# Optimization experiments

Hardware: AMD Instinct MI355X
Metric: run time of the kernel (lower is better)

Reference implementation:

```python
import jax, jax.numpy as jnp
import numpy as np

B, N, M, DN, DE, WN, WE, P = 16, 128, 1024, 512, 256, 128, 128, 512
EMB = WN + WE            # nenn embedding size per node / per edge
CLS_IN = 2 * EMB // 1    # = 2*wn + 2*we = 512
LR_OUT, CR_OUT, MR_OUT = 9, 6, 17
HID = 256


def _mk_params(key):
    ks = jax.random.split(key, 16)
    s = 0.02
    p = {
        'Wn':  jax.random.normal(ks[0], (DN, WN), jnp.float32) * s,
        'We':  jax.random.normal(ks[1], (DE, WE), jnp.float32) * s,
        'Wn2': jax.random.normal(ks[2], (DN, WN), jnp.float32) * s,
        'We2': jax.random.normal(ks[3], (DE, WE), jnp.float32) * s,
    }
    for i, h in enumerate(['scr', 'lr', 'mr']):
        out = {'scr': CR_OUT, 'lr': LR_OUT, 'mr': MR_OUT}[h]
        p[h + '_W1'] = jax.random.normal(ks[4 + 4 * i], (2 * EMB, HID), jnp.float32) * s
        p[h + '_b1'] = jnp.zeros((HID,), jnp.float32)
        p[h + '_W2'] = jax.random.normal(ks[5 + 4 * i], (HID, out), jnp.float32) * s
        p[h + '_b2'] = jnp.zeros((out,), jnp.float32)
    return p


def setup_inputs() -> dict:
    key = jax.random.key(0)
    ks = jax.random.split(key, 10)
    inp = {
        'node_features': jax.random.normal(ks[0], (B, N, DN), jnp.float32),
        'edge_features': jax.random.normal(ks[1], (B, N, N, DE), jnp.float32),
        'adj_mat': (jax.random.uniform(ks[2], (B, N, N)) < 0.1).astype(jnp.float32),
        'line_adj_mat': (jax.random.uniform(ks[3], (B, M, M)) < 0.02).astype(jnp.float32),
        'edge_index': jax.random.randint(ks[4], (B, 2, M), 0, N, jnp.int32),
        'object_pairs': jax.random.randint(ks[5], (B, P, 2), 0, N, jnp.int32),
        'num_obj': jax.random.randint(ks[6], (B,), N // 4, N + 1, jnp.int32),
        'num_edges': jax.random.randint(ks[7], (B,), M // 4, M + 1, jnp.int32),
    }
    inp.update(_mk_params(ks[8]))
    return inp


def _mlp(x, W1, b1, W2, b2):
    return jax.nn.relu(x @ W1 + b1) @ W2 + b2


def _forward(node_features, edge_features, adj_mat, line_adj_mat,
             Wn, We, Wn2, We2,
             scr_W1, scr_b1, scr_W2, scr_b2,
             lr_W1, lr_b1, lr_W2, lr_b2,
             mr_W1, mr_b1, mr_W2, mr_b2,
             edge_index, object_pairs, num_obj, num_edges):
    dt = node_features.dtype
    # ragged slicing [:num_obj] / [:num_edges] expressed as masks (padding stays 0)
    nmask = (jnp.arange(N) < num_obj[:, None]).astype(dt)      # [B,N]
    emask = (jnp.arange(M) < num_edges[:, None]).astype(dt)    # [B,M]

    X = node_features * nmask[..., None]                        # [B,N,DN]
    A = (adj_mat * nmask[:, :, None] * nmask[:, None, :]
         + jnp.eye(N, dtype=dt)[None] * nmask[:, :, None])      # A + I, masked
    h = jax.nn.relu((A @ X) @ Wn) * nmask[..., None]            # [B,N,WN] node-level emb

    src, dst = edge_index[:, 0], edge_index[:, 1]               # [B,M]
    Eg = jax.vmap(lambda e, s, d: e[s, d])(edge_features, src, dst)  # [B,M,DE]
    Eg = Eg * emask[..., None]
    L = (line_adj_mat * emask[:, :, None] * emask[:, None, :]
         + jnp.eye(M, dtype=dt)[None] * emask[:, :, None])      # line graph A + I
    g = jax.nn.relu((L @ Eg) @ We) * emask[..., None]           # [B,M,WE] edge-level emb

    # aggregate edge embeddings onto their source nodes (ragged scatter-add)
    agg = jax.vmap(lambda gb, sb: jnp.zeros((N, WE), gb.dtype).at[sb].add(gb))(g, src)
    node_emb = jnp.concatenate([h, agg * nmask[..., None]], -1)  # [B,N,EMB]

    # dense pairwise edge embeddings [B,N,N,EMB]
    Xp = X @ Wn2                                                 # [B,N,WN]
    Pm = jax.nn.relu(Xp[:, :, None, :] + Xp[:, None, :, :])      # node part [B,N,N,WN]
    Q = jax.nn.relu(edge_features @ We2)                         # edge part [B,N,N,WE]
    edge_emb = jnp.concatenate([Pm, Q], -1)

    # make_classifier_inputs: fused ragged gather instead of python double loop
    p0, p1 = object_pairs[..., 0], object_pairs[..., 1]          # [B,P]
    emb0 = jnp.take_along_axis(node_emb, p0[:, :, None], axis=1)  # [B,P,EMB]
    emb1 = jnp.take_along_axis(node_emb, p1[:, :, None], axis=1)
    eedge = jax.vmap(lambda eb, a, b: eb[a, b])(edge_emb, p0, p1)  # [B,P,EMB]
    ci = jnp.concatenate([emb0 + emb1, eedge], -1)               # aggregator='sum'

    lr = _mlp(ci, lr_W1, lr_b1, lr_W2, lr_b2)
    cr = _mlp(ci, scr_W1, scr_b1, scr_W2, scr_b2)
    mr = _mlp(ci, mr_W1, mr_b1, mr_W2, mr_b2)
    return lr, cr, mr


def reference(node_features, edge_features, adj_mat, line_adj_mat,
              edge_index, object_pairs, num_obj, num_edges,
              Wn, We, Wn2, We2,
              scr_W1, scr_b1, scr_W2, scr_b2,
              lr_W1, lr_b1, lr_W2, lr_b2,
              mr_W1, mr_b1, mr_W2, mr_b2):
    return _forward(node_features, edge_features, adj_mat, line_adj_mat,
                    Wn, We, Wn2, We2,
                    scr_W1, scr_b1, scr_W2, scr_b2,
                    lr_W1, lr_b1, lr_W2, lr_b2,
                    mr_W1, mr_b1, mr_W2, mr_b2,
                    edge_index, object_pairs, num_obj, num_edges)
```

## Files before the change

kernel.cpp:

```cpp
#include <hip/hip_runtime.h>
#include <hip/hip_bf16.h>
#include <cstdint>
#include <cstddef>

#define BB 16
#define NN 128
#define MM 1024
#define DN 512
#define DE 256
#define WN 128
#define WE 128
#define PP 512
#define HIDW 256
#define CIW 512

typedef __attribute__((ext_vector_type(8))) short s16x8;
typedef __attribute__((ext_vector_type(4))) float f32x4;

__device__ __forceinline__ float bf2f(unsigned short u) {
    unsigned int x = ((unsigned int)u) << 16;
    union { unsigned int i; float f; } c; c.i = x; return c.f;
}
__device__ __forceinline__ short f2b(float f) {
    __hip_bfloat16 h = __float2bfloat16(f);
    return *reinterpret_cast<short*>(&h);
}

__global__ __launch_bounds__(256) void k0_prep(
    const float* __restrict__ lrW1, const float* __restrict__ scrW1,
    const float* __restrict__ mrW1,
    const float* __restrict__ lrb1, const float* __restrict__ scrb1,
    const float* __restrict__ mrb1,
    const float* __restrict__ Wn, const float* __restrict__ Wn2,
    const float* __restrict__ We, const float* __restrict__ We2,
    __hip_bfloat16* __restrict__ W1t, __hip_bfloat16* __restrict__ WncT,
    __hip_bfloat16* __restrict__ WeT, __hip_bfloat16* __restrict__ We2T,
    float* __restrict__ b1cat)
{
    int blk = blockIdx.x;
    int t = threadIdx.x;
    if (blk < 768) {
        int h = blk >> 8, n = blk & 255;
        const float* W = (h == 0) ? lrW1 : (h == 1) ? scrW1 : mrW1;
        W1t[(size_t)blk * 512 + t]       = __float2bfloat16(W[t * 256 + n]);
        W1t[(size_t)blk * 512 + t + 256] = __float2bfloat16(W[(t + 256) * 256 + n]);
    } else if (blk == 768) {
        b1cat[t]       = lrb1[t];
        b1cat[256 + t] = scrb1[t];
        b1cat[512 + t] = mrb1[t];
    } else if (blk < 897) {
        int n = blk - 769;
        WeT[(size_t)n * 256 + t] = __float2bfloat16(We[t * 128 + n]);
    } else if (blk < 1153) {
        int n = blk - 897;
        const float* W = (n < 128) ? Wn : Wn2;
        int c = n & 127;
        WncT[(size_t)n * 512 + t]       = __float2bfloat16(W[t * 128 + c]);
        WncT[(size_t)n * 512 + t + 256] = __float2bfloat16(W[(t + 256) * 128 + c]);
    } else {
        int n = blk - 1153;
        We2T[(size_t)n * 256 + t] = __float2bfloat16(We2[t * 128 + n]);
    }
}

__global__ __launch_bounds__(256) void fproj(
    const float* __restrict__ nf, const float* __restrict__ ef,
    const int* __restrict__ eidx, const int* __restrict__ opair,
    const int* __restrict__ nobj, const int* __restrict__ nedg,
    const ushort* __restrict__ WncT, const ushort* __restrict__ WeT,
    const ushort* __restrict__ We2T,
    float* __restrict__ Y, float* __restrict__ Xp,
    float* __restrict__ G1, __hip_bfloat16* __restrict__ ci)
{
    __shared__ ushort As[128 * 32];
    __shared__ ushort Bs[128 * 32];
    __shared__ unsigned rowoff[128];
    __shared__ float    rowval[128];

    int blk = blockIdx.x;
    int route, mb, nb, K;
    const ushort* Bt;
    if (blk < 32)       { route = 0; mb = blk >> 1;  nb = blk & 1; K = 512; Bt = WncT; }
    else if (blk < 160) { route = 1; mb = blk - 32;  nb = 0;       K = 256; Bt = WeT;  }
    else                { route = 2; mb = blk - 160; nb = 0;       K = 256; Bt = We2T; }
    int row0 = mb * 128, col0 = nb * 128;
    int t = threadIdx.x;

    if (t < 128) {
        int r = row0 + t;
        unsigned off; float valid = 1.f;
        if (route == 0) {
            int b = r >> 7, i = r & 127;
            off = (unsigned)r * DN;
            valid = (i < nobj[b]) ? 1.f : 0.f;
        } else if (route == 1) {
            int b = r >> 10, m = r & 1023;
            int src = eidx[b * 2 * MM + m];
            int dst = eidx[b * 2 * MM + MM + m];
            off = (unsigned)((b * NN + src) * NN + dst) * DE;
            valid = (m < nedg[b]) ? 1.f : 0.f;
        } else {
            int r2 = r;
            int b = r2 >> 9, p = r2 & 511;
            int i0 = opair[(b * PP + p) * 2];
            int i1 = opair[(b * PP + p) * 2 + 1];
            off = (unsigned)((b * NN + i0) * NN + i1) * DE;
        }
        rowoff[t] = off; rowval[t] = valid;
    }

    const float* Asrc = (route == 0) ? nf : ef;
    int lane = t & 63;
    int w    = t >> 6;
    int wr   = w >> 1, wc = w & 1;
    int arow = w * 32 + (lane >> 2);
    int ak   = (lane & 3) * 8;
    int qk   = (lane >> 4) * 8;
    int fr   = lane & 15;
    f32x4 acc[4][4];
    #pragma unroll
    for (int i = 0; i < 4; ++i)
        #pragma unroll
        for (int j = 0; j < 4; ++j) acc[i][j] = (f32x4){0.f, 0.f, 0.f, 0.f};

    for (int k0 = 0; k0 < K; k0 += 32) {
        __syncthreads();
        {
            unsigned o0 = rowoff[arow] + k0 + ak;
            unsigned o1 = rowoff[arow + 16] + k0 + ak;
            float m0 = rowval[arow], m1 = rowval[arow + 16];
            float4 a0 = *(const float4*)&Asrc[o0];
            float4 a1 = *(const float4*)&Asrc[o0 + 4];
            float4 b0 = *(const float4*)&Asrc[o1];
            float4 b1 = *(const float4*)&Asrc[o1 + 4];
            s16x8 pa, pb;
            pa[0]=f2b(a0.x*m0); pa[1]=f2b(a0.y*m0); pa[2]=f2b(a0.z*m0); pa[3]=f2b(a0.w*m0);
            pa[4]=f2b(a1.x*m0); pa[5]=f2b(a1.y*m0); pa[6]=f2b(a1.z*m0); pa[7]=f2b(a1.w*m0);
            pb[0]=f2b(b0.x*m1); pb[1]=f2b(b0.y*m1); pb[2]=f2b(b0.z*m1); pb[3]=f2b(b0.w*m1);
            pb[4]=f2b(b1.x*m1); pb[5]=f2b(b1.y*m1); pb[6]=f2b(b1.z*m1); pb[7]=f2b(b1.w*m1);
            *(s16x8*)&As[arow * 32 + ak]        = pa;
            *(s16x8*)&As[(arow + 16) * 32 + ak] = pb;
            *(s16x8*)&Bs[arow * 32 + ak] =
                *(const s16x8*)&Bt[(size_t)(col0 + arow) * K + k0 + ak];
            *(s16x8*)&Bs[(arow + 16) * 32 + ak] =
                *(const s16x8*)&Bt[(size_t)(col0 + arow + 16) * K + k0 + ak];
        }
        __syncthreads();
        s16x8 af[4], bfv[4];
        #pragma unroll
        for (int mi = 0; mi < 4; ++mi)
            af[mi] = *(const s16x8*)&As[(wr * 64 + mi * 16 + fr) * 32 + qk];
        #pragma unroll
        for (int ni = 0; ni < 4; ++ni)
            bfv[ni] = *(const s16x8*)&Bs[(wc * 64 + ni * 16 + fr) * 32 + qk];
        #pragma unroll
        for (int mi = 0; mi < 4; ++mi)
            #pragma unroll
            for (int ni = 0; ni < 4; ++ni)
                acc[mi][ni] = __builtin_amdgcn_mfma_f32_16x16x32_bf16(
                    af[mi], bfv[ni], acc[mi][ni], 0, 0, 0);
    }
    int crow = (lane >> 4) * 4;
    #pragma unroll
    for (int mi = 0; mi < 4; ++mi) {
        #pragma unroll
        for (int ni = 0; ni < 4; ++ni) {
            int gc = col0 + wc * 64 + ni * 16 + fr;
            int gr = row0 + wr * 64 + mi * 16 + crow;
            #pragma unroll
            for (int rg = 0; rg < 4; ++rg) {
                float v = acc[mi][ni][rg];
                int r = gr + rg;
                if (route == 0) {
                    if (gc < 128) Y [(size_t)r * WN + gc]       = v;
                    else          Xp[(size_t)r * WN + gc - 128] = v;
                } else if (route == 1) {
                    G1[(size_t)r * WE + gc] = v;
                } else {
                    ci[(size_t)r * CIW + 384 + gc] = __float2bfloat16(fmaxf(v, 0.f));
                }
            }
        }
    }
}

__global__ __launch_bounds__(256) void k2_gcn_node(
    const float* __restrict__ adj, const int* __restrict__ num_obj,
    const float* __restrict__ Y, float* __restrict__ node_emb)
{
    __shared__ float As[16 * 129];
    int b  = blockIdx.x >> 4;
    int i0 = ((blockIdx.x >> 1) & 7) * 16;
    int ch = blockIdx.x & 1;
    int s  = num_obj[b];
    int t  = threadIdx.x;
    if (t < 128) {
        for (int rr = 0; rr < 16; ++rr) {
            int i = i0 + rr;
            float v = 0.f;
            if (i < s) {
                v = adj[(size_t)(b * NN + i) * NN + t] * ((t < s) ? 1.f : 0.f);
                if (t == i) v += 1.f;
            }
            As[rr * 129 + t] = v;
        }
    }
    __syncthreads();
    int c  = ch * 64 + (t & 63);
    int rb = (t >> 6) * 4;
    float acc[4] = {0.f,0.f,0.f,0.f};
    for (int j = 0; j < NN; ++j) {
        float yv = Y[(b * NN + j) * WN + c];
        #pragma unroll
        for (int r = 0; r < 4; ++r) acc[r] += As[(rb + r) * 129 + j] * yv;
    }
    #pragma unroll
    for (int r = 0; r < 4; ++r) {
        int i = i0 + rb + r;
        node_emb[(b * NN + i) * 256 + c]       = fmaxf(acc[r], 0.f);
        node_emb[(b * NN + i) * 256 + 128 + c] = 0.f;
    }
}

__global__ __launch_bounds__(128) void k4_line_gcn(
    const float* __restrict__ la, const float* __restrict__ G1,
    const int* __restrict__ eidx, const int* __restrict__ num_edges,
    float* __restrict__ node_emb)
{
    int b = blockIdx.x >> 10;
    int m = blockIdx.x & 1023;
    int se = num_edges[b];
    if (m >= se) return;
    __shared__ int   cnt;
    __shared__ int   idxs[MM];
    __shared__ float vals[MM];
    int t = threadIdx.x;
    if (t == 0) cnt = 0;
    __syncthreads();
    const float* larow = la + ((size_t)b * MM + m) * MM;
    for (int it = 0; it < 8; ++it) {
        int j = it * 128 + t;
        float v = larow[j];
        if (v != 0.f) {
            int pos = atomicAdd(&cnt, 1);
            idxs[pos] = j;
            vals[pos] = v;
        }
    }
    __syncthreads();
    int n = cnt;
    const float* g1b = G1 + (size_t)b * MM * WE;
    float acc = g1b[m * WE + t];
    for (int p = 0; p < n; ++p)
        acc += vals[p] * g1b[idxs[p] * WE + t];
    float g = fmaxf(acc, 0.f);
    int src = eidx[b * 2 * MM + m];
    atomicAdd(&node_emb[(b * NN + src) * 256 + 128 + t], g);
}

__global__ __launch_bounds__(256) void k5a_build_ci(
    const float* __restrict__ node_emb, const float* __restrict__ Xp,
    const int* __restrict__ opairs, const int* __restrict__ num_obj,
    __hip_bfloat16* __restrict__ ci)
{
    __shared__ int   pi0[16], pi1[16];
    __shared__ float nm0[16], nm1[16];
    int b     = blockIdx.x >> 5;
    int pbase = (blockIdx.x & 31) * 16;
    int t     = threadIdx.x;
    int s     = num_obj[b];
    if (t < 16) {
        int p  = pbase + t;
        int i0 = opairs[(b * PP + p) * 2];
        int i1 = opairs[(b * PP + p) * 2 + 1];
        pi0[t] = i0; pi1[t] = i1;
        nm0[t] = (i0 < s) ? 1.f : 0.f;
        nm1[t] = (i1 < s) ? 1.f : 0.f;
    }
    __syncthreads();
    for (int pp = 0; pp < 16; ++pp) {
        int i0 = pi0[pp], i1 = pi1[pp];
        int p  = pbase + pp;
        __hip_bfloat16* cirow = ci + (size_t)(b * PP + p) * CIW;
        float m0f = (t < 128) ? 1.f : nm0[pp];
        float m1f = (t < 128) ? 1.f : nm1[pp];
        float v = node_emb[(b * NN + i0) * 256 + t] * m0f
                + node_emb[(b * NN + i1) * 256 + t] * m1f;
        cirow[t] = __float2bfloat16(v);
        if (t < 128) {
            float pm = Xp[(b * NN + i0) * WN + t] + Xp[(b * NN + i1) * WN + t];
            cirow[256 + t] = __float2bfloat16(fmaxf(pm, 0.f));
        }
    }
}

__global__ __launch_bounds__(256) void k6_mlp1_mfma(
    const ushort* __restrict__ A,
    const ushort* __restrict__ Bt,
    const float* __restrict__ b1cat,
    __hip_bfloat16* __restrict__ H)
{
    __shared__ ushort As[128 * 32];
    __shared__ ushort Bs[128 * 32];
    int t    = threadIdx.x;
    int col0 = blockIdx.x * 128;
    int row0 = blockIdx.y * 128;
    int lane = t & 63;
    int w    = t >> 6;
    int wr   = w >> 1, wc = w & 1;
    int arow = w * 32 + (lane >> 2);
    int ak   = (lane & 3) * 8;
    int qk   = (lane >> 4) * 8;
    int fr   = lane & 15;
    f32x4 acc[4][4];
    #pragma unroll
    for (int i = 0; i < 4; ++i)
        #pragma unroll
        for (int j = 0; j < 4; ++j) acc[i][j] = (f32x4){0.f, 0.f, 0.f, 0.f};

    for (int k0 = 0; k0 < CIW; k0 += 32) {
        __syncthreads();
        *(s16x8*)&As[arow * 32 + ak] =
            *(const s16x8*)&A[(size_t)(row0 + arow) * CIW + k0 + ak];
        *(s16x8*)&As[(arow + 16) * 32 + ak] =
            *(const s16x8*)&A[(size_t)(row0 + arow + 16) * CIW + k0 + ak];
        *(s16x8*)&Bs[arow * 32 + ak] =
            *(const s16x8*)&Bt[(size_t)(col0 + arow) * CIW + k0 + ak];
        *(s16x8*)&Bs[(arow + 16) * 32 + ak] =
            *(const s16x8*)&Bt[(size_t)(col0 + arow + 16) * CIW + k0 + ak];
        __syncthreads();
        s16x8 af[4], bfv[4];
        #pragma unroll
        for (int mi = 0; mi < 4; ++mi)
            af[mi] = *(const s16x8*)&As[(wr * 64 + mi * 16 + fr) * 32 + qk];
        #pragma unroll
        for (int ni = 0; ni < 4; ++ni)
            bfv[ni] = *(const s16x8*)&Bs[(wc * 64 + ni * 16 + fr) * 32 + qk];
        #pragma unroll
        for (int mi = 0; mi < 4; ++mi)
            #pragma unroll
            for (int ni = 0; ni < 4; ++ni)
                acc[mi][ni] = __builtin_amdgcn_mfma_f32_16x16x32_bf16(
                    af[mi], bfv[ni], acc[mi][ni], 0, 0, 0);
    }
    int crow = (lane >> 4) * 4;
    #pragma unroll
    for (int mi = 0; mi < 4; ++mi) {
        #pragma unroll
        for (int ni = 0; ni < 4; ++ni) {
            int gc = col0 + wc * 64 + ni * 16 + fr;
            int gr = row0 + wr * 64 + mi * 16 + crow;
            float bias = b1cat[gc];
            #pragma unroll
            for (int rg = 0; rg < 4; ++rg) {
                float v = fmaxf(acc[mi][ni][rg] + bias, 0.f);
                H[(size_t)(gr + rg) * 768 + gc] = __float2bfloat16(v);
            }
        }
    }
}

__global__ __launch_bounds__(256) void k7_mlp2(
    const __hip_bfloat16* __restrict__ H,
    const float* __restrict__ lrW2, const float* __restrict__ lrb2,
    const float* __restrict__ scrW2, const float* __restrict__ scrb2,
    const float* __restrict__ mrW2, const float* __restrict__ mrb2,
    float* __restrict__ outp)
{
    __shared__ float w2s[32 * 257];
    int t = threadIdx.x;
    for (int o = 0; o < 32; ++o) {
        float v;
        if (o < 9)       v = lrW2[t * 9 + o];
        else if (o < 15) v = scrW2[t * 6 + (o - 9)];
        else             v = mrW2[t * 17 + (o - 15)];
        w2s[o * 257 + t] = v;
    }
    __syncthreads();
    int p = blockIdx.x * 8 + (t >> 5);
    int o = t & 31;
    int seg = (o < 9) ? 0 : ((o < 15) ? 1 : 2);
    const ushort* hr = (const ushort*)H + (size_t)p * 768 + seg * 256;
    const float* wr = &w2s[o * 257];
    float acc = (o < 9) ? lrb2[o] : ((o < 15) ? scrb2[o - 9] : mrb2[o - 15]);
    for (int k = 0; k < HIDW; k += 2) {
        ushort2 u = *(const ushort2*)&hr[k];
        acc += bf2f(u.x) * wr[k] + bf2f(u.y) * wr[k + 1];
    }
    if (o < 9)       outp[(size_t)p * 9 + o] = acc;
    else if (o < 15) outp[8192 * 9 + (size_t)p * 6 + (o - 9)] = acc;
    else             outp[8192 * 15 + (size_t)p * 17 + (o - 15)] = acc;
}

extern "C" void kernel_launch(void* const* d_in, const int* in_sizes, int n_in,
                              void* d_out, int out_size, void* d_ws, size_t ws_size,
                              hipStream_t stream) {
    const float* nf    = (const float*)d_in[0];
    const float* ef    = (const float*)d_in[1];
    const float* adj   = (const float*)d_in[2];
    const float* la    = (const float*)d_in[3];
    const int*   eidx  = (const int*)d_in[4];
    const int*   opair = (const int*)d_in[5];
    const int*   nobj  = (const int*)d_in[6];
    const int*   nedg  = (const int*)d_in[7];
    const float* Wn    = (const float*)d_in[8];
    const float* We    = (const float*)d_in[9];
    const float* Wn2   = (const float*)d_in[10];
    const float* We2   = (const float*)d_in[11];
    const float* scrW1 = (const float*)d_in[12];
    const float* scrb1 = (const float*)d_in[13];
    const float* scrW2 = (const float*)d_in[14];
    const float* scrb2 = (const float*)d_in[15];
    const float* lrW1  = (const float*)d_in[16];
    const float* lrb1  = (const float*)d_in[17];
    const float* lrW2  = (const float*)d_in[18];
    const float* lrb2  = (const float*)d_in[19];
    const float* mrW1  = (const float*)d_in[20];
    const float* mrb1  = (const float*)d_in[21];
    const float* mrW2  = (const float*)d_in[22];
    const float* mrb2  = (const float*)d_in[23];

    float* ws = (float*)d_ws;
    float* Y        = ws;
    float* Xp       = Y + 262144;
    float* node_emb = Xp + 262144;
    float* G1       = node_emb + 524288;
    float* base     = G1 + 2097152;
    __hip_bfloat16* ci   = (__hip_bfloat16*)base;
    __hip_bfloat16* hid  = (__hip_bfloat16*)(base + 2097152);
    __hip_bfloat16* W1t  = (__hip_bfloat16*)(base + 2097152 + 3145728);
    __hip_bfloat16* WncT = (__hip_bfloat16*)(base + 2097152 + 3145728 + 196608);
    __hip_bfloat16* WeT  = (__hip_bfloat16*)(base + 2097152 + 3145728 + 196608 + 65536);
    __hip_bfloat16* We2T = (__hip_bfloat16*)(base + 2097152 + 3145728 + 196608 + 65536 + 16384);
    float* b1cat = base + 2097152 + 3145728 + 196608 + 65536 + 16384 + 16384;

    k0_prep <<<1281, 256, 0, stream>>>(lrW1, scrW1, mrW1, lrb1, scrb1, mrb1,
                                       Wn, Wn2, We, We2,
                                       W1t, WncT, WeT, We2T, b1cat);
    fproj   <<<224, 256, 0, stream>>>(nf, ef, eidx, opair, nobj, nedg,
                                      (const ushort*)WncT, (const ushort*)WeT,
                                      (const ushort*)We2T, Y, Xp, G1, ci);
    k2_gcn_node <<<BB * 8 * 2, 256, 0, stream>>>(adj, nobj, Y, node_emb);
    k4_line_gcn <<<BB * MM, 128, 0, stream>>>(la, G1, eidx, nedg, node_emb);
    k5a_build_ci<<<BB * (PP / 16), 256, 0, stream>>>(node_emb, Xp, opair, nobj, ci);
    k6_mlp1_mfma<<<dim3(6, 64), 256, 0, stream>>>((const ushort*)ci,
                                                  (const ushort*)W1t, b1cat, hid);
    k7_mlp2     <<<8192 / 8, 256, 0, stream>>>(hid, lrW2, lrb2, scrW2, scrb2,
                                               mrW2, mrb2, (float*)d_out);
}
```

Before: 475.0 us.

## Move GCN, line-GCN and MLP2 onto bf16 MFMA and fuse ci build into MLP1

The node GCN and the line-graph GCN become dense bf16 MFMA GEMMs over the adjacency matrices, with masking and self-loops applied while loading tiles. This replaces the per-edge sparse gather loop, which launched 16K blocks. The pair-feature construction (k5a) is folded into the MLP1 A-tile loader, and the second MLP layer becomes an MFMA GEMM against a padded concatenated W2. Intermediates Y and G1 are stored transposed in bf16. The costs are dense work on a sparse line adjacency (1024x1024 per batch) and extra bf16 rounding of the adjacency values and intermediates.

```diff
diff --git a/kernel.cpp b/kernel.cpp
--- a/kernel.cpp
+++ b/kernel.cpp
@@ -8,22 +8,15 @@
 #define MM 1024
 #define DN 512
 #define DE 256
-#define WN 128
-#define WE 128
 #define PP 512
-#define HIDW 256
-#define CIW 512
 
 typedef __attribute__((ext_vector_type(8))) short s16x8;
 typedef __attribute__((ext_vector_type(4))) float f32x4;
-
-__device__ __forceinline__ float bf2f(unsigned short u) {
-    unsigned int x = ((unsigned int)u) << 16;
-    union { unsigned int i; float f; } c; c.i = x; return c.f;
-}
-__device__ __forceinline__ short f2b(float f) {
+typedef __attribute__((ext_vector_type(4))) unsigned short u16x4;
+
+__device__ __forceinline__ unsigned short f2b(float f) {
     __hip_bfloat16 h = __float2bfloat16(f);
-    return *reinterpret_cast<short*>(&h);
+    return *reinterpret_cast<unsigned short*>(&h);
 }
 
 __global__ __launch_bounds__(256) void k0_prep(
@@ -33,33 +26,52 @@
     const float* __restrict__ mrb1,
     const float* __restrict__ Wn, const float* __restrict__ Wn2,
     const float* __restrict__ We, const float* __restrict__ We2,
-    __hip_bfloat16* __restrict__ W1t, __hip_bfloat16* __restrict__ WncT,
-    __hip_bfloat16* __restrict__ WeT, __hip_bfloat16* __restrict__ We2T,
-    float* __restrict__ b1cat)
+    const float* __restrict__ lrW2, const float* __restrict__ scrW2,
+    const float* __restrict__ mrW2,
+    const float* __restrict__ lrb2, const float* __restrict__ scrb2,
+    const float* __restrict__ mrb2,
+    ushort* __restrict__ W1t, ushort* __restrict__ WncT,
+    ushort* __restrict__ WeT, ushort* __restrict__ We2T,
+    ushort* __restrict__ W2catB,
+    float* __restrict__ b1cat, float* __restrict__ b2cat)
 {
     int blk = blockIdx.x;
     int t = threadIdx.x;
     if (blk < 768) {
         int h = blk >> 8, n = blk & 255;
         const float* W = (h == 0) ? lrW1 : (h == 1) ? scrW1 : mrW1;
-        W1t[(size_t)blk * 512 + t]       = __float2bfloat16(W[t * 256 + n]);
-        W1t[(size_t)blk * 512 + t + 256] = __float2bfloat16(W[(t + 256) * 256 + n]);
+        W1t[(size_t)blk * 512 + t]       = f2b(W[t * 256 + n]);
+        W1t[(size_t)blk * 512 + t + 256] = f2b(W[(t + 256) * 256 + n]);
     } else if (blk == 768) {
         b1cat[t]       = lrb1[t];
         b1cat[256 + t] = scrb1[t];
         b1cat[512 + t] = mrb1[t];
     } else if (blk < 897) {
         int n = blk - 769;
-        WeT[(size_t)n * 256 + t] = __float2bfloat16(We[t * 128 + n]);
+        WeT[(size_t)n * 256 + t] = f2b(We[t * 128 + n]);
     } else if (blk < 1153) {
         int n = blk - 897;
         const float* W = (n < 128) ? Wn : Wn2;
         int c = n & 127;
-        WncT[(size_t)n * 512 + t]       = __float2bfloat16(W[t * 128 + c]);
-        WncT[(size_t)n * 512 + t + 256] = __float2bfloat16(W[(t + 256) * 128 + c]);
+        WncT[(size_t)n * 512 + t]       = f2b(W[t * 128 + c]);
+        WncT[(size_t)n * 512 + t + 256] = f2b(W[(t + 256) * 128 + c]);
+    } else if (blk < 1281) {
+        int n = blk - 1153;
+        We2T[(size_t)n * 256 + t] = f2b(We2[t * 128 + n]);
+    } else if (blk < 1313) {
+        int o = blk - 1281;
+        for (int i = 0; i < 3; ++i) {
+            int k = i * 256 + t;
+            int seg = k >> 8, kk = k & 255;
+            float v = 0.f;
+            if (o < 9)       { if (seg == 0) v = lrW2[kk * 9 + o]; }
+            else if (o < 15) { if (seg == 1) v = scrW2[kk * 6 + (o - 9)]; }
+            else             { if (seg == 2) v = mrW2[kk * 17 + (o - 15)]; }
+            W2catB[(size_t)o * 768 + k] = f2b(v);
+        }
     } else {
-        int n = blk - 1153;
-        We2T[(size_t)n * 256 + t] = __float2bfloat16(We2[t * 128 + n]);
+        if (t < 32)
+            b2cat[t] = (t < 9) ? lrb2[t] : (t < 15) ? scrb2[t - 9] : mrb2[t - 15];
     }
 }
 
@@ -69,8 +81,8 @@
     const int* __restrict__ nobj, const int* __restrict__ nedg,
     const ushort* __restrict__ WncT, const ushort* __restrict__ WeT,
     const ushort* __restrict__ We2T,
-    float* __restrict__ Y, float* __restrict__ Xp,
-    float* __restrict__ G1, __hip_bfloat16* __restrict__ ci)
+    ushort* __restrict__ Yt, float* __restrict__ Xp,
+    ushort* __restrict__ G1t, ushort* __restrict__ ci2)
 {
     __shared__ ushort As[128 * 32];
     __shared__ ushort Bs[128 * 32];
@@ -100,8 +112,7 @@
             off = (unsigned)((b * NN + src) * NN + dst) * DE;
             valid = (m < nedg[b]) ? 1.f : 0.f;
         } else {
-            int r2 = r;
-            int b = r2 >> 9, p = r2 & 511;
+            int b = r >> 9, p = r & 511;
             int i0 = opair[(b * PP + p) * 2];
             int i1 = opair[(b * PP + p) * 2 + 1];
             off = (unsigned)((b * NN + i0) * NN + i1) * DE;
@@ -165,169 +176,261 @@
     for (int mi = 0; mi < 4; ++mi) {
         #pragma unroll
         for (int ni = 0; ni < 4; ++ni) {
-            int gc = col0 + wc * 64 + ni * 16 + fr;
-            int gr = row0 + wr * 64 + mi * 16 + crow;
-            #pragma unroll
-            for (int rg = 0; rg < 4; ++rg) {
-                float v = acc[mi][ni][rg];
-                int r = gr + rg;
-                if (route == 0) {
-                    if (gc < 128) Y [(size_t)r * WN + gc]       = v;
-                    else          Xp[(size_t)r * WN + gc - 128] = v;
-                } else if (route == 1) {
-                    G1[(size_t)r * WE + gc] = v;
-                } else {
-                    ci[(size_t)r * CIW + 384 + gc] = __float2bfloat16(fmaxf(v, 0.f));
-                }
+            int c   = wc * 64 + ni * 16 + fr;
+            int lr0 = wr * 64 + mi * 16 + crow;
+            if (route == 0 && nb == 0) {
+                u16x4 pk;
+                #pragma unroll
+                for (int rg = 0; rg < 4; ++rg) pk[rg] = f2b(acc[mi][ni][rg]);
+                *(u16x4*)&Yt[(size_t)mb * 16384 + c * 128 + lr0] = pk;
+            } else if (route == 0) {
+                #pragma unroll
+                for (int rg = 0; rg < 4; ++rg)
+                    Xp[(size_t)(row0 + lr0 + rg) * 128 + c] = acc[mi][ni][rg];
+            } else if (route == 1) {
+                int r0 = row0 + lr0;
+                int b1 = r0 >> 10, m0 = r0 & 1023;
+                u16x4 pk;
+                #pragma unroll
+                for (int rg = 0; rg < 4; ++rg) pk[rg] = f2b(acc[mi][ni][rg]);
+                *(u16x4*)&G1t[(size_t)b1 * 131072 + c * 1024 + m0] = pk;
+            } else {
+                #pragma unroll
+                for (int rg = 0; rg < 4; ++rg)
+                    ci2[(size_t)(row0 + lr0 + rg) * 128 + c] =
+                        f2b(fmaxf(acc[mi][ni][rg], 0.f));
             }
         }
     }
 }
 
-__global__ __launch_bounds__(256) void k2_gcn_node(
-    const float* __restrict__ adj, const int* __restrict__ num_obj,
-    const float* __restrict__ Y, float* __restrict__ node_emb)
-{
-    __shared__ float As[16 * 129];
-    int b  = blockIdx.x >> 4;
-    int i0 = ((blockIdx.x >> 1) & 7) * 16;
-    int ch = blockIdx.x & 1;
-    int s  = num_obj[b];
-    int t  = threadIdx.x;
-    if (t < 128) {
-        for (int rr = 0; rr < 16; ++rr) {
-            int i = i0 + rr;
-            float v = 0.f;
-            if (i < s) {
-                v = adj[(size_t)(b * NN + i) * NN + t] * ((t < s) ? 1.f : 0.f);
-                if (t == i) v += 1.f;
-            }
-            As[rr * 129 + t] = v;
-        }
-    }
-    __syncthreads();
-    int c  = ch * 64 + (t & 63);
-    int rb = (t >> 6) * 4;
-    float acc[4] = {0.f,0.f,0.f,0.f};
-    for (int j = 0; j < NN; ++j) {
-        float yv = Y[(b * NN + j) * WN + c];
-        #pragma unroll
-        for (int r = 0; r < 4; ++r) acc[r] += As[(rb + r) * 129 + j] * yv;
-    }
-    #pragma unroll
-    for (int r = 0; r < 4; ++r) {
-        int i = i0 + rb + r;
-        node_emb[(b * NN + i) * 256 + c]       = fmaxf(acc[r], 0.f);
-        node_emb[(b * NN + i) * 256 + 128 + c] = 0.f;
-    }
-}
-
-__global__ __launch_bounds__(128) void k4_line_gcn(
-    const float* __restrict__ la, const float* __restrict__ G1,
-    const int* __restrict__ eidx, const int* __restrict__ num_edges,
-    float* __restrict__ node_emb)
-{
-    int b = blockIdx.x >> 10;
-    int m = blockIdx.x & 1023;
-    int se = num_edges[b];
-    if (m >= se) return;
-    __shared__ int   cnt;
-    __shared__ int   idxs[MM];
-    __shared__ float vals[MM];
-    int t = threadIdx.x;
-    if (t == 0) cnt = 0;
-    __syncthreads();
-    const float* larow = la + ((size_t)b * MM + m) * MM;
-    for (int it = 0; it < 8; ++it) {
-        int j = it * 128 + t;
-        float v = larow[j];
-        if (v != 0.f) {
-            int pos = atomicAdd(&cnt, 1);
-            idxs[pos] = j;
-            vals[pos] = v;
-        }
-    }
-    __syncthreads();
-    int n = cnt;
-    const float* g1b = G1 + (size_t)b * MM * WE;
-    float acc = g1b[m * WE + t];
-    for (int p = 0; p < n; ++p)
-        acc += vals[p] * g1b[idxs[p] * WE + t];
-    float g = fmaxf(acc, 0.f);
-    int src = eidx[b * 2 * MM + m];
-    atomicAdd(&node_emb[(b * NN + src) * 256 + 128 + t], g);
-}
-
-__global__ __launch_bounds__(256) void k5a_build_ci(
-    const float* __restrict__ node_emb, const float* __restrict__ Xp,
-    const int* __restrict__ opairs, const int* __restrict__ num_obj,
-    __hip_bfloat16* __restrict__ ci)
-{
-    __shared__ int   pi0[16], pi1[16];
-    __shared__ float nm0[16], nm1[16];
-    int b     = blockIdx.x >> 5;
-    int pbase = (blockIdx.x & 31) * 16;
-    int t     = threadIdx.x;
-    int s     = num_obj[b];
-    if (t < 16) {
-        int p  = pbase + t;
-        int i0 = opairs[(b * PP + p) * 2];
-        int i1 = opairs[(b * PP + p) * 2 + 1];
-        pi0[t] = i0; pi1[t] = i1;
-        nm0[t] = (i0 < s) ? 1.f : 0.f;
-        nm1[t] = (i1 < s) ? 1.f : 0.f;
-    }
-    __syncthreads();
-    for (int pp = 0; pp < 16; ++pp) {
-        int i0 = pi0[pp], i1 = pi1[pp];
-        int p  = pbase + pp;
-        __hip_bfloat16* cirow = ci + (size_t)(b * PP + p) * CIW;
-        float m0f = (t < 128) ? 1.f : nm0[pp];
-        float m1f = (t < 128) ? 1.f : nm1[pp];
-        float v = node_emb[(b * NN + i0) * 256 + t] * m0f
-                + node_emb[(b * NN + i1) * 256 + t] * m1f;
-        cirow[t] = __float2bfloat16(v);
-        if (t < 128) {
-            float pm = Xp[(b * NN + i0) * WN + t] + Xp[(b * NN + i1) * WN + t];
-            cirow[256 + t] = __float2bfloat16(fmaxf(pm, 0.f));
-        }
-    }
-}
-
-__global__ __launch_bounds__(256) void k6_mlp1_mfma(
-    const ushort* __restrict__ A,
-    const ushort* __restrict__ Bt,
-    const float* __restrict__ b1cat,
-    __hip_bfloat16* __restrict__ H)
+__global__ __launch_bounds__(256) void k2m_gcn(
+    const float* __restrict__ adj, const int* __restrict__ nobj,
+    const ushort* __restrict__ Yt, float* __restrict__ node_emb)
 {
     __shared__ ushort As[128 * 32];
     __shared__ ushort Bs[128 * 32];
+    int b = blockIdx.x;
+    int s = nobj[b];
+    int t = threadIdx.x;
+    int lane = t & 63, w = t >> 6, wr = w >> 1, wc = w & 1;
+    int arow = w * 32 + (lane >> 2);
+    int ak   = (lane & 3) * 8;
+    int qk   = (lane >> 4) * 8, fr = lane & 15;
+    f32x4 acc[4][4];
+    #pragma unroll
+    for (int i = 0; i < 4; ++i)
+        #pragma unroll
+        for (int j = 0; j < 4; ++j) acc[i][j] = (f32x4){0.f, 0.f, 0.f, 0.f};
+
+    for (int k0 = 0; k0 < 128; k0 += 32) {
+        __syncthreads();
+        #pragma unroll
+        for (int rr = 0; rr < 2; ++rr) {
+            int i = arow + rr * 16;
+            float rm = (i < s) ? 1.f : 0.f;
+            const float* ar = adj + ((size_t)(b * NN + i)) * NN + k0 + ak;
+            float4 a0 = *(const float4*)ar;
+            float4 a1 = *(const float4*)(ar + 4);
+            float vv[8] = {a0.x,a0.y,a0.z,a0.w,a1.x,a1.y,a1.z,a1.w};
+            s16x8 pk;
+            #pragma unroll
+            for (int e = 0; e < 8; ++e) {
+                int j = k0 + ak + e;
+                float cm = (j < s) ? 1.f : 0.f;
+                float v = vv[e] * rm * cm + ((j == i) ? rm : 0.f);
+                pk[e] = (short)f2b(v);
+            }
+            *(s16x8*)&As[i * 32 + ak] = pk;
+            *(s16x8*)&Bs[i * 32 + ak] =
+                *(const s16x8*)&Yt[(size_t)b * 16384 + i * 128 + k0 + ak];
+        }
+        __syncthreads();
+        s16x8 af[4], bfv[4];
+        #pragma unroll
+        for (int mi = 0; mi < 4; ++mi)
+            af[mi] = *(const s16x8*)&As[(wr * 64 + mi * 16 + fr) * 32 + qk];
+        #pragma unroll
+        for (int ni = 0; ni < 4; ++ni)
+            bfv[ni] = *(const s16x8*)&Bs[(wc * 64 + ni * 16 + fr) * 32 + qk];
+        #pragma unroll
+        for (int mi = 0; mi < 4; ++mi)
+            #pragma unroll
+            for (int ni = 0; ni < 4; ++ni)
+                acc[mi][ni] = __builtin_amdgcn_mfma_f32_16x16x32_bf16(
+                    af[mi], bfv[ni], acc[mi][ni], 0, 0, 0);
+    }
+    int crow = (lane >> 4) * 4;
+    #pragma unroll
+    for (int mi = 0; mi < 4; ++mi) {
+        #pragma unroll
+        for (int ni = 0; ni < 4; ++ni) {
+            int gc = wc * 64 + ni * 16 + fr;
+            int i0 = wr * 64 + mi * 16 + crow;
+            #pragma unroll
+            for (int rg = 0; rg < 4; ++rg) {
+                node_emb[(size_t)(b * NN + i0 + rg) * 256 + gc] =
+                    fmaxf(acc[mi][ni][rg], 0.f);
+                node_emb[(size_t)(b * NN + i0 + rg) * 256 + 128 + gc] = 0.f;
+            }
+        }
+    }
+}
+
+__global__ __launch_bounds__(256) void lgemm(
+    const float* __restrict__ la, const ushort* __restrict__ G1t,
+    const int* __restrict__ eidx, const int* __restrict__ nedg,
+    float* __restrict__ node_emb)
+{
+    __shared__ ushort As[64 * 32];
+    __shared__ ushort Bs[128 * 32];
+    __shared__ int srcs[64];
+    int b  = blockIdx.x >> 4;
+    int mt = blockIdx.x & 15;
+    int row0 = mt * 64;
+    int se = nedg[b];
+    int t = threadIdx.x;
+    if (t < 64) srcs[t] = eidx[b * 2 * MM + row0 + t];
+    int lane = t & 63, w = t >> 6, wr = w >> 1, wc = w & 1;
+    int arow = t >> 2;
+    int ak   = (t & 3) * 8;
+    int qk   = (lane >> 4) * 8, fr = lane & 15;
+    f32x4 acc[2][4];
+    #pragma unroll
+    for (int i = 0; i < 2; ++i)
+        #pragma unroll
+        for (int j = 0; j < 4; ++j) acc[i][j] = (f32x4){0.f, 0.f, 0.f, 0.f};
+    const ushort* g1tb = G1t + (size_t)b * 131072;
+
+    for (int k0 = 0; k0 < 1024; k0 += 32) {
+        __syncthreads();
+        {
+            int m = row0 + arow;
+            float rm = (m < se) ? 1.f : 0.f;
+            const float* lr_ = la + ((size_t)(b * MM + m)) * MM + k0 + ak;
+            float4 a0 = *(const float4*)lr_;
+            float4 a1 = *(const float4*)(lr_ + 4);
+            float vv[8] = {a0.x,a0.y,a0.z,a0.w,a1.x,a1.y,a1.z,a1.w};
+            s16x8 pa;
+            #pragma unroll
+            for (int e = 0; e < 8; ++e) {
+                int j = k0 + ak + e;
+                float cm = (j < se) ? 1.f : 0.f;
+                float v = vv[e] * rm * cm + ((j == m) ? rm : 0.f);
+                pa[e] = (short)f2b(v);
+            }
+            *(s16x8*)&As[arow * 32 + ak] = pa;
+            *(s16x8*)&Bs[arow * 32 + ak] =
+                *(const s16x8*)&g1tb[(size_t)arow * 1024 + k0 + ak];
+            *(s16x8*)&Bs[(arow + 64) * 32 + ak] =
+                *(const s16x8*)&g1tb[(size_t)(arow + 64) * 1024 + k0 + ak];
+        }
+        __syncthreads();
+        s16x8 af[2], bfv[4];
+        #pragma unroll
+        for (int mi = 0; mi < 2; ++mi)
+            af[mi] = *(const s16x8*)&As[(wr * 32 + mi * 16 + fr) * 32 + qk];
+        #pragma unroll
+        for (int ni = 0; ni < 4; ++ni)
+            bfv[ni] = *(const s16x8*)&Bs[(wc * 64 + ni * 16 + fr) * 32 + qk];
+        #pragma unroll
+        for (int mi = 0; mi < 2; ++mi)
+            #pragma unroll
+            for (int ni = 0; ni < 4; ++ni)
+                acc[mi][ni] = __builtin_amdgcn_mfma_f32_16x16x32_bf16(
+                    af[mi], bfv[ni], acc[mi][ni], 0, 0, 0);
+    }
+    int crow = (lane >> 4) * 4;
+    #pragma unroll
+    for (int mi = 0; mi < 2; ++mi) {
+        #pragma unroll
+        for (int ni = 0; ni < 4; ++ni) {
+            int gc   = wc * 64 + ni * 16 + fr;
+            int lrow = wr * 32 + mi * 16 + crow;
+            #pragma unroll
+            for (int rg = 0; rg < 4; ++rg) {
+                float g = fmaxf(acc[mi][ni][rg], 0.f);
+                int node = srcs[lrow + rg];
+                atomicAdd(&node_emb[(size_t)(b * NN + node) * 256 + 128 + gc], g);
+            }
+        }
+    }
+}
+
+__global__ __launch_bounds__(256) void k6_mlp1(
+    const float* __restrict__ node_emb, const float* __restrict__ Xp,
+    const ushort* __restrict__ ci2, const ushort* __restrict__ W1t,
+    const float* __restrict__ b1cat,
+    const int* __restrict__ opair, const int* __restrict__ nobj,
+    ushort* __restrict__ H)
+{
+    __shared__ ushort As[128 * 32];
+    __shared__ ushort Bs[128 * 32];
+    __shared__ int po0[128], po1[128], px0[128], px1[128];
+    __shared__ float pn0[128], pn1[128];
     int t    = threadIdx.x;
     int col0 = blockIdx.x * 128;
     int row0 = blockIdx.y * 128;
-    int lane = t & 63;
-    int w    = t >> 6;
-    int wr   = w >> 1, wc = w & 1;
+    if (t < 128) {
+        int r = row0 + t;
+        int b = r >> 9, p = r & 511;
+        int i0 = opair[(b * PP + p) * 2];
+        int i1 = opair[(b * PP + p) * 2 + 1];
+        int s  = nobj[b];
+        po0[t] = (b * NN + i0) * 256;
+        po1[t] = (b * NN + i1) * 256;
+        px0[t] = (b * NN + i0) * 128;
+        px1[t] = (b * NN + i1) * 128;
+        pn0[t] = (i0 < s) ? 1.f : 0.f;
+        pn1[t] = (i1 < s) ? 1.f : 0.f;
+    }
+    int lane = t & 63, w = t >> 6, wr = w >> 1, wc = w & 1;
     int arow = w * 32 + (lane >> 2);
     int ak   = (lane & 3) * 8;
-    int qk   = (lane >> 4) * 8;
-    int fr   = lane & 15;
+    int qk   = (lane >> 4) * 8, fr = lane & 15;
     f32x4 acc[4][4];
     #pragma unroll
     for (int i = 0; i < 4; ++i)
         #pragma unroll
         for (int j = 0; j < 4; ++j) acc[i][j] = (f32x4){0.f, 0.f, 0.f, 0.f};
 
-    for (int k0 = 0; k0 < CIW; k0 += 32) {
-        __syncthreads();
-        *(s16x8*)&As[arow * 32 + ak] =
-            *(const s16x8*)&A[(size_t)(row0 + arow) * CIW + k0 + ak];
-        *(s16x8*)&As[(arow + 16) * 32 + ak] =
-            *(const s16x8*)&A[(size_t)(row0 + arow + 16) * CIW + k0 + ak];
+    for (int k0 = 0; k0 < 512; k0 += 32) {
+        __syncthreads();
+        #pragma unroll
+        for (int rr = 0; rr < 2; ++rr) {
+            int row = arow + rr * 16;
+            s16x8 pk;
+            if (k0 < 256) {
+                const float* pa = node_emb + po0[row] + k0 + ak;
+                const float* pb = node_emb + po1[row] + k0 + ak;
+                float4 a0 = *(const float4*)pa, a1 = *(const float4*)(pa + 4);
+                float4 b0 = *(const float4*)pb, b1 = *(const float4*)(pb + 4);
+                float m0 = (k0 >= 128) ? pn0[row] : 1.f;
+                float m1 = (k0 >= 128) ? pn1[row] : 1.f;
+                pk[0]=f2b(a0.x*m0+b0.x*m1); pk[1]=f2b(a0.y*m0+b0.y*m1);
+                pk[2]=f2b(a0.z*m0+b0.z*m1); pk[3]=f2b(a0.w*m0+b0.w*m1);
+                pk[4]=f2b(a1.x*m0+b1.x*m1); pk[5]=f2b(a1.y*m0+b1.y*m1);
+                pk[6]=f2b(a1.z*m0+b1.z*m1); pk[7]=f2b(a1.w*m0+b1.w*m1);
+            } else if (k0 < 384) {
+                int kk = k0 - 256 + ak;
+                const float* pa = Xp + px0[row] + kk;
+                const float* pb = Xp + px1[row] + kk;
+                float4 a0 = *(const float4*)pa, a1 = *(const float4*)(pa + 4);
+                float4 b0 = *(const float4*)pb, b1 = *(const float4*)(pb + 4);
+                pk[0]=f2b(fmaxf(a0.x+b0.x,0.f)); pk[1]=f2b(fmaxf(a0.y+b0.y,0.f));
+                pk[2]=f2b(fmaxf(a0.z+b0.z,0.f)); pk[3]=f2b(fmaxf(a0.w+b0.w,0.f));
+                pk[4]=f2b(fmaxf(a1.x+b1.x,0.f)); pk[5]=f2b(fmaxf(a1.y+b1.y,0.f));
+                pk[6]=f2b(fmaxf(a1.z+b1.z,0.f)); pk[7]=f2b(fmaxf(a1.w+b1.w,0.f));
+            } else {
+                int kk = k0 - 384 + ak;
+                pk = *(const s16x8*)&ci2[(size_t)(row0 + row) * 128 + kk];
+            }
+            *(s16x8*)&As[row * 32 + ak] = pk;
+        }
         *(s16x8*)&Bs[arow * 32 + ak] =
-            *(const s16x8*)&Bt[(size_t)(col0 + arow) * CIW + k0 + ak];
+            *(const s16x8*)&W1t[(size_t)(col0 + arow) * 512 + k0 + ak];
         *(s16x8*)&Bs[(arow + 16) * 32 + ak] =
-            *(const s16x8*)&Bt[(size_t)(col0 + arow + 16) * CIW + k0 + ak];
+            *(const s16x8*)&W1t[(size_t)(col0 + arow + 16) * 512 + k0 + ak];
         __syncthreads();
         s16x8 af[4], bfv[4];
         #pragma unroll
@@ -352,44 +455,59 @@
             int gr = row0 + wr * 64 + mi * 16 + crow;
             float bias = b1cat[gc];
             #pragma unroll
-            for (int rg = 0; rg < 4; ++rg) {
-                float v = fmaxf(acc[mi][ni][rg] + bias, 0.f);
-                H[(size_t)(gr + rg) * 768 + gc] = __float2bfloat16(v);
-            }
-        }
-    }
-}
-
-__global__ __launch_bounds__(256) void k7_mlp2(
-    const __hip_bfloat16* __restrict__ H,
-    const float* __restrict__ lrW2, const float* __restrict__ lrb2,
-    const float* __restrict__ scrW2, const float* __restrict__ scrb2,
-    const float* __restrict__ mrW2, const float* __restrict__ mrb2,
-    float* __restrict__ outp)
+            for (int rg = 0; rg < 4; ++rg)
+                H[(size_t)(gr + rg) * 768 + gc] =
+                    f2b(fmaxf(acc[mi][ni][rg] + bias, 0.f));
+        }
+    }
+}
+
+__global__ __launch_bounds__(256) void k8_mlp2(
+    const ushort* __restrict__ H, const ushort* __restrict__ W2catB,
+    const float* __restrict__ b2cat, float* __restrict__ outp)
 {
-    __shared__ float w2s[32 * 257];
+    __shared__ ushort As[64 * 32];
+    __shared__ ushort Bs[32 * 32];
     int t = threadIdx.x;
-    for (int o = 0; o < 32; ++o) {
-        float v;
-        if (o < 9)       v = lrW2[t * 9 + o];
-        else if (o < 15) v = scrW2[t * 6 + (o - 9)];
-        else             v = mrW2[t * 17 + (o - 15)];
-        w2s[o * 257 + t] = v;
-    }
-    __syncthreads();
-    int p = blockIdx.x * 8 + (t >> 5);
-    int o = t & 31;
-    int seg = (o < 9) ? 0 : ((o < 15) ? 1 : 2);
-    const ushort* hr = (const ushort*)H + (size_t)p * 768 + seg * 256;
-    const float* wr = &w2s[o * 257];
-    float acc = (o < 9) ? lrb2[o] : ((o < 15) ? scrb2[o - 9] : mrb2[o - 15]);
-    for (int k = 0; k < HIDW; k += 2) {
-        ushort2 u = *(const ushort2*)&hr[k];
-        acc += bf2f(u.x) * wr[k] + bf2f(u.y) * wr[k + 1];
-    }
-    if (o < 9)       outp[(size_t)p * 9 + o] = acc;
-    else if (o < 15) outp[8192 * 9 + (size_t)p * 6 + (o - 9)] = acc;
-    else             outp[8192 * 15 + (size_t)p * 17 + (o - 15)] = acc;
+    int row0 = blockIdx.x * 64;
+    int lane = t & 63, w = t >> 6;
+    int arow = t >> 2;
+    int ak   = (t & 3) * 8;
+    int qk   = (lane >> 4) * 8, fr = lane & 15;
+    f32x4 acc[2];
+    acc[0] = (f32x4){0.f,0.f,0.f,0.f};
+    acc[1] = (f32x4){0.f,0.f,0.f,0.f};
+    for (int k0 = 0; k0 < 768; k0 += 32) {
+        __syncthreads();
+        *(s16x8*)&As[arow * 32 + ak] =
+            *(const s16x8*)&H[(size_t)(row0 + arow) * 768 + k0 + ak];
+        if (t < 128) {
+            int br = t >> 2;
+            *(s16x8*)&Bs[br * 32 + ((t & 3) * 8)] =
+                *(const s16x8*)&W2catB[(size_t)br * 768 + k0 + (t & 3) * 8];
+        }
+        __syncthreads();
+        s16x8 af = *(const s16x8*)&As[(w * 16 + fr) * 32 + qk];
+        s16x8 b0 = *(const s16x8*)&Bs[fr * 32 + qk];
+        s16x8 b1 = *(const s16x8*)&Bs[(16 + fr) * 32 + qk];
+        acc[0] = __builtin_amdgcn_mfma_f32_16x16x32_bf16(af, b0, acc[0], 0, 0, 0);
+        acc[1] = __builtin_amdgcn_mfma_f32_16x16x32_bf16(af, b1, acc[1], 0, 0, 0);
+    }
+    int crow = (lane >> 4) * 4;
+    #pragma unroll
+    for (int ni = 0; ni < 2; ++ni) {
+        int o = ni * 16 + fr;
+        float bias = b2cat[o];
+        int gr = row0 + w * 16 + crow;
+        #pragma unroll
+        for (int rg = 0; rg < 4; ++rg) {
+            float v = acc[ni][rg] + bias;
+            int p = gr + rg;
+            if (o < 9)       outp[(size_t)p * 9 + o] = v;
+            else if (o < 15) outp[8192 * 9 + (size_t)p * 6 + (o - 9)] = v;
+            else             outp[8192 * 15 + (size_t)p * 17 + (o - 15)] = v;
+        }
+    }
 }
 
 extern "C" void kernel_launch(void* const* d_in, const int* in_sizes, int n_in,
@@ -421,30 +539,29 @@
     const float* mrb2  = (const float*)d_in[23];
 
     float* ws = (float*)d_ws;
-    float* Y        = ws;
-    float* Xp       = Y + 262144;
-    float* node_emb = Xp + 262144;
-    float* G1       = node_emb + 524288;
-    float* base     = G1 + 2097152;
-    __hip_bfloat16* ci   = (__hip_bfloat16*)base;
-    __hip_bfloat16* hid  = (__hip_bfloat16*)(base + 2097152);
-    __hip_bfloat16* W1t  = (__hip_bfloat16*)(base + 2097152 + 3145728);
-    __hip_bfloat16* WncT = (__hip_bfloat16*)(base + 2097152 + 3145728 + 196608);
-    __hip_bfloat16* WeT  = (__hip_bfloat16*)(base + 2097152 + 3145728 + 196608 + 65536);
-    __hip_bfloat16* We2T = (__hip_bfloat16*)(base + 2097152 + 3145728 + 196608 + 65536 + 16384);
-    float* b1cat = base + 2097152 + 3145728 + 196608 + 65536 + 16384 + 16384;
-
-    k0_prep <<<1281, 256, 0, stream>>>(lrW1, scrW1, mrW1, lrb1, scrb1, mrb1,
-                                       Wn, Wn2, We, We2,
-                                       W1t, WncT, WeT, We2T, b1cat);
-    fproj   <<<224, 256, 0, stream>>>(nf, ef, eidx, opair, nobj, nedg,
-                                      (const ushort*)WncT, (const ushort*)WeT,
-                                      (const ushort*)We2T, Y, Xp, G1, ci);
-    k2_gcn_node <<<BB * 8 * 2, 256, 0, stream>>>(adj, nobj, Y, node_emb);
-    k4_line_gcn <<<BB * MM, 128, 0, stream>>>(la, G1, eidx, nedg, node_emb);
-    k5a_build_ci<<<BB * (PP / 16), 256, 0, stream>>>(node_emb, Xp, opair, nobj, ci);
-    k6_mlp1_mfma<<<dim3(6, 64), 256, 0, stream>>>((const ushort*)ci,
-                                                  (const ushort*)W1t, b1cat, hid);
-    k7_mlp2     <<<8192 / 8, 256, 0, stream>>>(hid, lrW2, lrb2, scrW2, scrb2,
-                                               mrW2, mrb2, (float*)d_out);
-}
+    float*  Xp       = ws;
+    float*  node_emb = ws + 262144;
+    ushort* Yt       = (ushort*)(ws + 786432);
+    ushort* G1t      = (ushort*)(ws + 917504);
+    ushort* ci2      = (ushort*)(ws + 1966080);
+    ushort* H        = (ushort*)(ws + 2490368);
+    ushort* W1t      = (ushort*)(ws + 5636096);
+    ushort* WncT     = (ushort*)(ws + 5832704);
+    ushort* WeT      = (ushort*)(ws + 5898240);
+    ushort* We2T     = (ushort*)(ws + 5914624);
+    ushort* W2catB   = (ushort*)(ws + 5931008);
+    float*  b1cat    = ws + 5943296;
+    float*  b2cat    = ws + 5944064;
+
+    k0_prep<<<1314, 256, 0, stream>>>(lrW1, scrW1, mrW1, lrb1, scrb1, mrb1,
+                                      Wn, Wn2, We, We2,
+                                      lrW2, scrW2, mrW2, lrb2, scrb2, mrb2,
+                                      W1t, WncT, WeT, We2T, W2catB, b1cat, b2cat);
+    fproj  <<<224, 256, 0, stream>>>(nf, ef, eidx, opair, nobj, nedg,
+                                     WncT, WeT, We2T, Yt, Xp, G1t, ci2);
+    k2m_gcn<<<BB, 256, 0, stream>>>(adj, nobj, Yt, node_emb);
+    lgemm  <<<BB * 16, 256, 0, stream>>>(la, G1t, eidx, nedg, node_emb);
+    k6_mlp1<<<dim3(6, 64), 256, 0, stream>>>(node_emb, Xp, ci2, W1t, b1cat,
+                                             opair, nobj, H);
+    k8_mlp2<<<128, 256, 0, stream>>>(H, W2catB, b2cat, (float*)d_out);
+}
```

Result: no change. 478.1 us (+0.7%).
